# Performance work log

Measured on AMD Instinct MI355X. Metric: run time of the kernel, lower is better.

The kernel has to match this reference:

```python
import jax, jax.numpy as jnp
import numpy as np

B, T, N, D = 8, 12, 512, 128
K = 16                      # number of pattern clusters
GEO_H, SEM_H, T_H = 4, 2, 2
HD = D // (GEO_H + SEM_H + T_H)      # 16
SCALE = HD ** -0.5
GD, SD, TD = GEO_H * HD, SEM_H * HD, T_H * HD  # 64, 32, 32


def setup_inputs() -> dict:
    key = jax.random.key(0)
    ks = jax.random.split(key, 24)
    w = lambda k, o, i: jax.random.normal(k, (o, i), jnp.float32) * 0.02
    return {
        'x': jax.random.normal(ks[0], (B, T, N, D), jnp.float32),
        'x_patterns': jax.random.normal(ks[1], (B, T, N, D, 1), jnp.float32),
        'pattern_keys': jax.random.normal(ks[2], (K, D, 1), jnp.float32),
        'dynamic_adj': jax.random.normal(ks[3], (B, N, N), jnp.float32) * 0.1,
        'geo_mask': jax.random.randint(ks[4], (N, N), 0, 2).astype(bool),
        'sem_mask': jax.random.randint(ks[5], (N, N), 0, 2).astype(bool),
        't_qw': w(ks[6], TD, D), 't_kw': w(ks[7], TD, D), 't_vw': w(ks[8], TD, D),
        'geo_qw': w(ks[9], GD, D), 'geo_kw': w(ks[10], GD, D), 'geo_vw': w(ks[11], GD, D),
        'sem_qw': w(ks[12], SD, D), 'sem_kw': w(ks[13], SD, D), 'sem_vw': w(ks[14], SD, D),
        'pat_qw': w(ks[15], GD, D), 'pat_qb': jax.random.normal(ks[16], (GD,), jnp.float32) * 0.02,
        'pat_kw': w(ks[17], GD, D), 'pat_kb': jax.random.normal(ks[18], (GD,), jnp.float32) * 0.02,
        'pat_vw': w(ks[19], GD, D), 'pat_vb': jax.random.normal(ks[20], (GD,), jnp.float32) * 0.02,
        'proj_w': w(ks[21], D, D), 'proj_b': jax.random.normal(ks[22], (D,), jnp.float32) * 0.02,
    }


def reference(x, x_patterns, pattern_keys, dynamic_adj, geo_mask, sem_mask,
              t_qw, t_kw, t_vw, geo_qw, geo_kw, geo_vw, sem_qw, sem_kw, sem_vw,
              pat_qw, pat_qb, pat_kw, pat_kb, pat_vw, pat_vb, proj_w, proj_b):
    Bc, Tc, Nc, Dc = x.shape
    proj3 = lambda z, w: jnp.einsum('btnd,ed->btne', z, w)  # 1x1 conv over channels

    # ---- temporal branch: attention over T per node ----
    def t_heads(z):  # (B,T,N,TD) -> (B,N,h,T,hd)
        return z.transpose(0, 2, 1, 3).reshape(Bc, Nc, Tc, T_H, HD).transpose(0, 1, 3, 2, 4)
    tq, tk, tv = t_heads(proj3(x, t_qw)), t_heads(proj3(x, t_kw)), t_heads(proj3(x, t_vw))
    t_attn = jax.nn.softmax(jnp.einsum('bnhqd,bnhkd->bnhqk', tq, tk) * SCALE, axis=-1)
    t_x = jnp.einsum('bnhqk,bnhkd->bnhqd', t_attn, tv)
    t_x = t_x.transpose(0, 1, 3, 2, 4).reshape(Bc, Nc, Tc, TD).transpose(0, 2, 1, 3)  # (B,T,N,TD)

    # ---- geo branch: pattern attention augments geo_k ----
    geo_q, geo_k, geo_v = proj3(x, geo_qw), proj3(x, geo_kw), proj3(x, geo_vw)
    pq = x_patterns[..., 0] @ pat_qw.T + pat_qb          # (B,T,N,GD)
    pk = pattern_keys[..., 0] @ pat_kw.T + pat_kb        # (K,GD)
    pv = pattern_keys[..., 0] @ pat_vw.T + pat_vb        # (K,GD)
    p_attn = jax.nn.softmax(jnp.einsum('btne,ke->btnk', pq, pk) * SCALE, axis=-1)
    geo_k = geo_k + jnp.einsum('btnk,ke->btne', p_attn, pv)

    def s_heads(z, h):  # (B,T,N,h*hd) -> (B,T,h,N,hd)
        return z.reshape(Bc, Tc, Nc, h, HD).transpose(0, 1, 3, 2, 4)
    gq, gk, gv = s_heads(geo_q, GEO_H), s_heads(geo_k, GEO_H), s_heads(geo_v, GEO_H)
    g_attn = jnp.einsum('bthqd,bthkd->bthqk', gq, gk) * SCALE
    g_attn = g_attn + dynamic_adj[:, None, None]         # dynamic bias
    g_attn = jnp.where(geo_mask, -jnp.inf, g_attn)
    g_attn = jax.nn.softmax(g_attn, axis=-1)
    geo_x = jnp.einsum('bthqk,bthkd->bthqd', g_attn, gv)
    geo_x = geo_x.transpose(0, 1, 3, 2, 4).reshape(Bc, Tc, Nc, GD)

    # ---- semantic branch ----
    sq = s_heads(proj3(x, sem_qw), SEM_H)
    sk = s_heads(proj3(x, sem_kw), SEM_H)
    sv = s_heads(proj3(x, sem_vw), SEM_H)
    s_attn = jnp.einsum('bthqd,bthkd->bthqk', sq, sk) * SCALE
    s_attn = jnp.where(sem_mask, -jnp.inf, s_attn)
    s_attn = jax.nn.softmax(s_attn, axis=-1)
    sem_x = jnp.einsum('bthqk,bthkd->bthqd', s_attn, sv)
    sem_x = sem_x.transpose(0, 1, 3, 2, 4).reshape(Bc, Tc, Nc, SD)

    out = jnp.concatenate([t_x, geo_x, sem_x], axis=-1) @ proj_w.T + proj_b
    return out
```

## Files before the change

kernel.cpp:

```cpp
#include <hip/hip_runtime.h>
#include <hip/hip_bf16.h>

using bf16 = __hip_bfloat16;
typedef __attribute__((ext_vector_type(8))) short short8;
typedef __attribute__((ext_vector_type(4))) float f32x4;

#define Bc 8
#define Tc 12
#define Nc 512
#define Dc 128
#define T_Hc 2
#define GEO_Hc 4
#define SEM_Hc 2
#define HDc 16
#define SCALEc 0.25f

constexpr size_t TSZ = (size_t)Bc * Nc * T_Hc * Tc * HDc;
constexpr size_t GSZ = (size_t)Bc * Tc * GEO_Hc * Nc * HDc;
constexpr size_t SSZ = (size_t)Bc * Tc * SEM_Hc * Nc * HDc;
constexpr size_t CSZ = (size_t)Bc * Tc * Nc * Dc;
constexpr size_t H_TQ = 0;
constexpr size_t H_TK = H_TQ + TSZ;
constexpr size_t H_TV = H_TK + TSZ;
constexpr size_t H_GQ = H_TV + TSZ;
constexpr size_t H_GK = H_GQ + GSZ;
constexpr size_t H_GV = H_GK + GSZ;
constexpr size_t H_SQ = H_GV + GSZ;
constexpr size_t H_SK = H_SQ + SSZ;
constexpr size_t H_SV = H_SK + SSZ;
constexpr size_t H_CC = H_SV + SSZ;
constexpr size_t H_END = H_CC + CSZ;
constexpr size_t F_PK = (H_END + 1) / 2;
constexpr size_t F_PV = F_PK + 1024;
constexpr size_t F_FLAG = F_PV + 1024;
constexpr size_t H_W2X = 2 * (F_FLAG + 64);
constexpr size_t H_W2O = H_W2X + 384 * 256;
constexpr size_t H_BG = H_TQ;
constexpr size_t H_BS = H_TQ + 2097152;

__device__ __forceinline__ float b2f(bf16 v) { return __bfloat162float(v); }
__device__ __forceinline__ bf16 f2b(float v) { return __float2bfloat16(v); }
__device__ __forceinline__ short f2bs(float v) {
    bf16 b = __float2bfloat16(v);
    return *reinterpret_cast<short*>(&b);
}
__device__ __forceinline__ float bs2f(short s) {
    union { unsigned u; float f; } x;
    x.u = ((unsigned)(unsigned short)s) << 16;
    return x.f;
}

__global__ __launch_bounds__(256) void k_prep(
    const float* __restrict__ pattern_keys, const float* __restrict__ pat_kw,
    const float* __restrict__ pat_kb, const float* __restrict__ pat_vw,
    const float* __restrict__ pat_vb, float* __restrict__ fws) {
    int idx = blockIdx.x * 256 + threadIdx.x;
    int which = idx >> 10;
    int r = idx & 1023;
    int k = r >> 6, e = r & 63;
    const float4* w = (const float4*)((which ? pat_vw : pat_kw) + (size_t)e * 128);
    const float4* pk = (const float4*)(pattern_keys + (size_t)k * 128);
    float acc = which ? pat_vb[e] : pat_kb[e];
#pragma unroll
    for (int j = 0; j < 32; ++j) {
        float4 a = pk[j], b = w[j];
        acc = fmaf(a.x, b.x, acc); acc = fmaf(a.y, b.y, acc);
        acc = fmaf(a.z, b.z, acc); acc = fmaf(a.w, b.w, acc);
    }
    fws[(which ? F_PV : F_PK) + (size_t)k * 64 + e] = acc;
}

__global__ __launch_bounds__(256) void k_maskdet(
    const unsigned char* __restrict__ mask, float* __restrict__ fws) {
    __shared__ int s_u8, s_odd4;
    int tid = threadIdx.x;
    if (tid == 0) { s_u8 = 0; s_odd4 = 0; }
    __syncthreads();
    int u8 = 0, odd4 = 0;
    for (int i = tid * 16; i < tid * 16 + 16; ++i) {
        unsigned char v = mask[i];
        if (v && (i & 3)) u8 = 1;
        if (v && ((i & 7) == 4)) odd4 = 1;
    }
    if (u8) atomicOr(&s_u8, 1);
    if (odd4) atomicOr(&s_odd4, 1);
    __syncthreads();
    if (tid == 0) fws[F_FLAG] = s_u8 ? 0.f : (s_odd4 ? 1.f : 2.f);
}

__device__ __forceinline__ const float* wrow(
    int gc, const float* tq, const float* tk, const float* tv,
    const float* gq, const float* gk, const float* gv,
    const float* sq, const float* sk, const float* sv) {
    if (gc < 32) return tq + (size_t)gc * 128;
    if (gc < 64) return tk + (size_t)(gc - 32) * 128;
    if (gc < 96) return tv + (size_t)(gc - 64) * 128;
    if (gc < 160) return gq + (size_t)(gc - 96) * 128;
    if (gc < 224) return gk + (size_t)(gc - 160) * 128;
    if (gc < 288) return gv + (size_t)(gc - 224) * 128;
    if (gc < 320) return sq + (size_t)(gc - 288) * 128;
    if (gc < 352) return sk + (size_t)(gc - 320) * 128;
    return sv + (size_t)(gc - 352) * 128;
}

__global__ __launch_bounds__(256) void k_wcvt(
    const float* __restrict__ t_qw, const float* __restrict__ t_kw,
    const float* __restrict__ t_vw, const float* __restrict__ geo_qw,
    const float* __restrict__ geo_kw, const float* __restrict__ geo_vw,
    const float* __restrict__ sem_qw, const float* __restrict__ sem_kw,
    const float* __restrict__ sem_vw, const float* __restrict__ proj_w,
    bf16* __restrict__ hb) {
    int gid = blockIdx.x * 256 + threadIdx.x;
    if (gid < 49152) {
        int row = gid >> 7, k = gid & 127;
        const float* src = wrow(row, t_qw, t_kw, t_vw, geo_qw, geo_kw, geo_vw,
                                sem_qw, sem_kw, sem_vw);
        float v = src[k];
        if ((row >= 96 && row < 160) || (row >= 288 && row < 320)) v *= SCALEc;
        bf16 bv = f2b(v);
        hb[H_W2X + (size_t)row * 256 + 2 * k] = bv;
        hb[H_W2X + (size_t)row * 256 + 2 * k + 1] = bv;
    } else {
        int g = gid - 49152;
        hb[H_W2O + g] = f2b(proj_w[g]);
    }
}

__global__ __launch_bounds__(256) void k_bias(
    const float* __restrict__ dyn, const unsigned char* __restrict__ gm,
    const unsigned char* __restrict__ sm, const float* __restrict__ fws,
    bf16* __restrict__ hb) {
    size_t gid = (size_t)blockIdx.x * 256 + threadIdx.x;
    int mode = (int)fws[F_FLAG];
    if (gid < 2097152) {
        size_t rem = gid & 262143;
        int mv = (mode == 0) ? (int)gm[rem]
               : (mode == 1) ? ((const int*)gm)[rem]
                             : ((const int*)gm)[2 * rem];
        hb[H_BG + gid] = f2b(mv ? -1e30f : dyn[gid]);
    } else if (gid < 2097152 + 262144) {
        size_t sid = gid - 2097152;
        int mv = (mode == 0) ? (int)sm[sid]
               : (mode == 1) ? ((const int*)sm)[sid]
                             : ((const int*)sm)[2 * sid];
        hb[H_BS + sid] = f2b(mv ? -1e30f : 0.f);
    }
}

__global__ __launch_bounds__(256, 2) void k_projx(
    const float* __restrict__ x, bf16* __restrict__ hb) {
    __shared__ short xs[128 * 256];

    int tid = threadIdx.x;
    int m0 = blockIdx.x * 128;
    int b = m0 / (Tc * Nc);
    int rr = m0 - b * Tc * Nc;
    int t = rr >> 9;
    int n0 = rr & 511;

    for (int u = tid; u < 4096; u += 256) {
        int row = u >> 5, g = u & 31;
        float4 v = *(const float4*)(x + (size_t)(m0 + row) * 128 + g * 4);
        short8 s;
        short h0 = f2bs(v.x); s[0] = h0; s[1] = f2bs(v.x - bs2f(h0));
        short h1 = f2bs(v.y); s[2] = h1; s[3] = f2bs(v.y - bs2f(h1));
        short h2 = f2bs(v.z); s[4] = h2; s[5] = f2bs(v.z - bs2f(h2));
        short h3 = f2bs(v.w); s[6] = h3; s[7] = f2bs(v.w - bs2f(h3));
        *(short8*)&xs[row * 256 + ((g ^ (row & 7)) << 3)] = s;
    }
    __syncthreads();

    int w = tid >> 6;
    int lane = tid & 63;
    int l15 = lane & 15;
    int quad = lane >> 4;
    const bf16* w2 = hb + H_W2X;

    for (int nc = 0; nc < 6; ++nc) {
        f32x4 acc[2][4];
#pragma unroll
        for (int i = 0; i < 2; ++i)
#pragma unroll
            for (int j = 0; j < 4; ++j) acc[i][j] = (f32x4){0.f, 0.f, 0.f, 0.f};

#pragma unroll
        for (int ks = 0; ks < 8; ++ks) {
            int r0 = w * 32 + l15;
            int r1 = r0 + 16;
            short8 a0 = *(const short8*)&xs[r0 * 256 + (((ks * 4 + quad) ^ (r0 & 7)) << 3)];
            short8 a1 = *(const short8*)&xs[r1 * 256 + (((ks * 4 + quad) ^ (r1 & 7)) << 3)];
#pragma unroll
            for (int nj = 0; nj < 4; ++nj) {
                short8 bfr = *(const short8*)(w2 + (size_t)(nc * 64 + nj * 16 + l15) * 256
                                              + ks * 32 + quad * 8);
                acc[0][nj] = __builtin_amdgcn_mfma_f32_16x16x32_bf16(a0, bfr, acc[0][nj], 0, 0, 0);
                acc[1][nj] = __builtin_amdgcn_mfma_f32_16x16x32_bf16(a1, bfr, acc[1][nj], 0, 0, 0);
            }
        }
#pragma unroll
        for (int nj = 0; nj < 4; ++nj) {
            int gc = nc * 64 + nj * 16 + l15;
            int tile16 = nc * 4 + nj;
            int d = gc & 15;
#pragma unroll
            for (int i = 0; i < 2; ++i) {
                int nrow0 = n0 + w * 32 + i * 16 + quad * 4;
#pragma unroll
                for (int r = 0; r < 4; ++r) {
                    int n = nrow0 + r;
                    float v = acc[i][nj][r];
                    size_t idx;
                    if (tile16 < 6) {
                        int which = gc >> 5, hh = (gc >> 4) & 1;
                        size_t base = which == 0 ? H_TQ : which == 1 ? H_TK : H_TV;
                        idx = base + ((size_t)(b * Nc + n) * T_Hc + hh) * (Tc * HDc)
                              + t * HDc + d;
                    } else if (tile16 < 18) {
                        int r2 = gc - 96;
                        int which = r2 >> 6, h = (r2 >> 4) & 3;
                        size_t base = which == 0 ? H_GQ : which == 1 ? H_GK : H_GV;
                        idx = base + (((size_t)b * Tc + t) * GEO_Hc + h) * (Nc * HDc)
                              + n * HDc + d;
                    } else {
                        int r2 = gc - 288;
                        int which = r2 >> 5, h = (r2 >> 4) & 1;
                        size_t base = which == 0 ? H_SQ : which == 1 ? H_SK : H_SV;
                        idx = base + (((size_t)b * Tc + t) * SEM_Hc + h) * (Nc * HDc)
                              + n * HDc + d;
                    }
                    hb[idx] = f2b(v);
                }
            }
        }
    }
}

__global__ __launch_bounds__(256, 2) void k_projp(
    const float* __restrict__ xp, const float* __restrict__ pat_qw,
    const float* __restrict__ pat_qb, const float* __restrict__ fws,
    bf16* __restrict__ hb) {
    __shared__ float xs[64 * 132];
    __shared__ float wsh[64 * 68];
    __shared__ float pks[1024], pvs[1024], pqbs[64];

    int tid = threadIdx.x;
    int tok0 = blockIdx.x * 64;
    int ty = tid >> 4, tx = tid & 15;

    for (int u = tid; u < 2048; u += 256) {
        int row = u >> 5, f4 = u & 31;
        *(float4*)&xs[row * 132 + f4 * 4] =
            *(const float4*)(xp + (size_t)(tok0 + row) * 128 + f4 * 4);
    }
    for (int u = tid; u < 1024; u += 256) {
        pks[u] = fws[F_PK + u];
        pvs[u] = fws[F_PV + u];
    }
    if (tid < 64) pqbs[tid] = pat_qb[tid];

    float acc[4][4] = {};
    for (int kh = 0; kh < 2; ++kh) {
        __syncthreads();
        for (int u = tid; u < 1024; u += 256) {
            int row = u >> 4, f4 = u & 15;
            *(float4*)&wsh[row * 68 + f4 * 4] =
                *(const float4*)(pat_qw + (size_t)row * 128 + kh * 64 + f4 * 4);
        }
        __syncthreads();
#pragma unroll 4
        for (int kk = 0; kk < 64; kk += 4) {
            float4 a[4], b[4];
#pragma unroll
            for (int i = 0; i < 4; ++i)
                a[i] = *(const float4*)&xs[(ty + 16 * i) * 132 + kh * 64 + kk];
#pragma unroll
            for (int j = 0; j < 4; ++j)
                b[j] = *(const float4*)&wsh[(tx + 16 * j) * 68 + kk];
#pragma unroll
            for (int i = 0; i < 4; ++i)
#pragma unroll
                for (int j = 0; j < 4; ++j) {
                    acc[i][j] = fmaf(a[i].x, b[j].x, acc[i][j]);
                    acc[i][j] = fmaf(a[i].y, b[j].y, acc[i][j]);
                    acc[i][j] = fmaf(a[i].z, b[j].z, acc[i][j]);
                    acc[i][j] = fmaf(a[i].w, b[j].w, acc[i][j]);
                }
        }
    }
    __syncthreads();
    float* pqs = xs;
    float* plogs = wsh;
#pragma unroll
    for (int i = 0; i < 4; ++i)
#pragma unroll
        for (int j = 0; j < 4; ++j)
            pqs[(ty + 16 * i) * 68 + tx + 16 * j] = acc[i][j] + pqbs[tx + 16 * j];
    __syncthreads();
    {
        int tok = tid >> 2, k4 = (tid & 3) * 4;
        for (int k = k4; k < k4 + 4; ++k) {
            float s = 0.f;
#pragma unroll 16
            for (int e = 0; e < 64; ++e)
                s = fmaf(pqs[tok * 68 + e], pks[k * 64 + e], s);
            plogs[tok * 17 + k] = s * SCALEc;
        }
    }
    __syncthreads();
    {
        int tok = tid >> 2, q = tid & 3;
        float mx = -1e30f;
        for (int k = 0; k < 16; ++k) mx = fmaxf(mx, plogs[tok * 17 + k]);
        float p[16], sum = 0.f;
        for (int k = 0; k < 16; ++k) {
            p[k] = __expf(plogs[tok * 17 + k] - mx);
            sum += p[k];
        }
        float inv = 1.f / sum;
        int token = tok0 + tok;
        int b = token / (Tc * Nc);
        int rr = token - b * Tc * Nc;
        int t = rr >> 9;
        int n = rr & 511;
        for (int cc = 0; cc < 16; ++cc) {
            int c = q * 16 + cc;
            float v = 0.f;
            for (int k = 0; k < 16; ++k) v = fmaf(p[k], pvs[k * 64 + c], v);
            v *= inv;
            size_t idx = H_GK + (((size_t)b * Tc + t) * GEO_Hc + (c >> 4)) * (Nc * HDc)
                         + n * HDc + (c & 15);
            hb[idx] = f2b(b2f(hb[idx]) + v);
        }
    }
}

__global__ __launch_bounds__(64) void k_tattn(bf16* __restrict__ hb) {
    int blk = blockIdx.x;
    int h = blk & 1;
    int bn = blk >> 1;
    int b = bn >> 9;
    int n = bn & 511;
    size_t base = ((size_t)(b * Nc + n) * T_Hc + h) * (Tc * HDc);

    __shared__ float q[192], kk[192], v[192], s[144];
    int tid = threadIdx.x;
    for (int u = tid; u < 192; u += 64) {
        q[u] = b2f(hb[H_TQ + base + u]);
        kk[u] = b2f(hb[H_TK + base + u]);
        v[u] = b2f(hb[H_TV + base + u]);
    }
    __syncthreads();
    for (int idx = tid; idx < 144; idx += 64) {
        int qi = idx / 12, ki = idx - qi * 12;
        float acc = 0.f;
#pragma unroll
        for (int d = 0; d < 16; ++d) acc = fmaf(q[qi * 16 + d], kk[ki * 16 + d], acc);
        s[idx] = acc * SCALEc;
    }
    __syncthreads();
    if (tid < 12) {
        float mx = -1e30f;
        for (int ki = 0; ki < 12; ++ki) mx = fmaxf(mx, s[tid * 12 + ki]);
        float sum = 0.f;
        for (int ki = 0; ki < 12; ++ki) {
            float p = __expf(s[tid * 12 + ki] - mx);
            s[tid * 12 + ki] = p;
            sum += p;
        }
        float inv = 1.f / sum;
        for (int ki = 0; ki < 12; ++ki) s[tid * 12 + ki] *= inv;
    }
    __syncthreads();
    for (int idx = tid; idx < 192; idx += 64) {
        int qi = idx >> 4, d = idx & 15;
        float acc = 0.f;
#pragma unroll
        for (int ki = 0; ki < 12; ++ki) acc = fmaf(s[qi * 12 + ki], v[ki * 16 + d], acc);
        hb[H_CC + (((size_t)b * Tc + qi) * Nc + n) * Dc + h * HDc + d] = f2b(acc);
    }
}

__global__ __launch_bounds__(256, 4) void k_attn2(
    bf16* __restrict__ hb, size_t QO, size_t KO, size_t VO, int H,
    const bf16* __restrict__ biasp, size_t bstride, int coff) {
    __shared__ short vt[16 * 512];
    __shared__ short pbuf[4][16 * 128];
    __shared__ float lt[4][16];
    __shared__ float at[4][16];

    int bid = blockIdx.x;
    int part = bid & 3;
    int bth_lin = bid >> 2;
    int h = bth_lin % H;
    int rest = bth_lin / H;
    int t = rest % Tc;
    int b = rest / Tc;

    size_t bth = (((size_t)b * Tc + t) * H + h) * (size_t)(Nc * HDc);
    const bf16* Qp = hb + QO + bth;
    const bf16* Kp = hb + KO + bth;
    const bf16* Vp = hb + VO + bth;
    const bf16* bp = biasp + (size_t)b * bstride;

    int tid = threadIdx.x;
    int w = tid >> 6;
    int lane = tid & 63;
    int l15 = lane & 15;
    int quad = lane >> 4;

    for (int idx = tid; idx < 8192; idx += 256) {
        int k = idx >> 4, d = idx & 15;
        int kk = ((((k >> 3) & 7) ^ (d & 7)) << 3) | (k & ~63) | (k & 7);
        vt[d * 512 + kk] = *reinterpret_cast<const short*>(Vp + idx);
    }
    __syncthreads();

    short* pw = &pbuf[w][0];
    float* lw = lt[w];
    float* aw = at[w];
    int sw = l15 & 7;

    for (int qq = 0; qq < 2; ++qq) {
        int q0 = part * 128 + w * 32 + qq * 16;
        int qg = q0 + l15;
        short8 bq = {0, 0, 0, 0, 0, 0, 0, 0};
        if (quad < 2) bq = *(const short8*)(Qp + (size_t)qg * 16 + quad * 8);

        float m_i = -3e38f, l_i = 0.f;
        f32x4 O = {0.f, 0.f, 0.f, 0.f};

        for (int ch = 0; ch < 4; ++ch) {
            int kabs0 = ch * 128;
            f32x4 S[8];
#pragma unroll
            for (int kt = 0; kt < 8; ++kt) {
                int kabs = kabs0 + kt * 16;
                short4 bb = *(const short4*)(bp + (size_t)qg * 512 + kabs + quad * 4);
                f32x4 c;
                c[0] = bs2f(bb.x); c[1] = bs2f(bb.y);
                c[2] = bs2f(bb.z); c[3] = bs2f(bb.w);
                short8 ak = {0, 0, 0, 0, 0, 0, 0, 0};
                if (quad < 2)
                    ak = *(const short8*)(Kp + (size_t)(kabs + l15) * 16 + quad * 8);
                S[kt] = __builtin_amdgcn_mfma_f32_16x16x32_bf16(ak, bq, c, 0, 0, 0);
            }
            float cm = S[0][0];
#pragma unroll
            for (int kt = 0; kt < 8; ++kt)
#pragma unroll
                for (int r = 0; r < 4; ++r) cm = fmaxf(cm, S[kt][r]);
            cm = fmaxf(cm, __shfl_xor(cm, 16));
            cm = fmaxf(cm, __shfl_xor(cm, 32));
            float mnew = fmaxf(m_i, cm);
            float alpha = __expf(m_i - mnew);
            m_i = mnew;
            float psum = 0.f;
#pragma unroll
            for (int kt = 0; kt < 8; ++kt) {
#pragma unroll
                for (int r = 0; r < 4; ++r) {
                    float p = __expf(S[kt][r] - mnew);
                    S[kt][r] = p;
                    psum += p;
                }
            }
            psum += __shfl_xor(psum, 16);
            psum += __shfl_xor(psum, 32);
            l_i = l_i * alpha + psum;
            if (quad == 0) aw[l15] = alpha;
#pragma unroll
            for (int kt = 0; kt < 8; ++kt) {
                short4 pk4;
                pk4.x = f2bs(S[kt][0]); pk4.y = f2bs(S[kt][1]);
                pk4.z = f2bs(S[kt][2]); pk4.w = f2bs(S[kt][3]);
                int g = 2 * kt + (quad >> 1);
                *(short4*)&pw[l15 * 128 + ((g ^ sw) << 3) + ((quad & 1) << 2)] = pk4;
            }
            float4 a4 = *(float4*)&aw[quad * 4];
            O[0] *= a4.x; O[1] *= a4.y; O[2] *= a4.z; O[3] *= a4.w;
#pragma unroll
            for (int kw = 0; kw < 4; ++kw) {
                int g = 4 * kw + quad;
                short8 ap = *(const short8*)&pw[l15 * 128 + ((g ^ sw) << 3)];
                short8 bv = *(const short8*)&vt[l15 * 512 + kabs0 + ((g ^ sw) << 3)];
                O = __builtin_amdgcn_mfma_f32_16x16x32_bf16(ap, bv, O, 0, 0, 0);
            }
        }
        if (quad == 0) lw[l15] = l_i;
        float4 l4 = *(float4*)&lw[quad * 4];
        float inv0 = 1.f / l4.x, inv1 = 1.f / l4.y, inv2 = 1.f / l4.z, inv3 = 1.f / l4.w;
        size_t obase = H_CC + (((size_t)b * Tc + t) * Nc + q0) * Dc + coff + h * HDc + l15;
        hb[obase + (size_t)(quad * 4 + 0) * Dc] = f2b(O[0] * inv0);
        hb[obase + (size_t)(quad * 4 + 1) * Dc] = f2b(O[1] * inv1);
        hb[obase + (size_t)(quad * 4 + 2) * Dc] = f2b(O[2] * inv2);
        hb[obase + (size_t)(quad * 4 + 3) * Dc] = f2b(O[3] * inv3);
    }
}

__global__ __launch_bounds__(256, 3) void k_outm(
    const bf16* __restrict__ hb, const float* __restrict__ proj_b,
    float* __restrict__ out) {
    __shared__ short cs[128 * 128];
    __shared__ float pbs[128];

    int tid = threadIdx.x;
    int m0 = blockIdx.x * 128;

    for (int u = tid; u < 2048; u += 256) {
        int row = u >> 4, g = u & 15;
        *(short8*)&cs[row * 128 + ((g ^ (row & 7)) << 3)] =
            *(const short8*)(hb + H_CC + (size_t)(m0 + row) * 128 + g * 8);
    }
    if (tid < 128) pbs[tid] = proj_b[tid];
    __syncthreads();

    int w = tid >> 6;
    int lane = tid & 63;
    int l15 = lane & 15;
    int quad = lane >> 4;
    const bf16* w2o = hb + H_W2O;

    f32x4 acc[2][8];
#pragma unroll
    for (int i = 0; i < 2; ++i)
#pragma unroll
        for (int j = 0; j < 8; ++j) acc[i][j] = (f32x4){0.f, 0.f, 0.f, 0.f};

#pragma unroll
    for (int ks = 0; ks < 4; ++ks) {
        int r0 = w * 32 + l15;
        int r1 = r0 + 16;
        short8 a0 = *(const short8*)&cs[r0 * 128 + (((ks * 4 + quad) ^ (r0 & 7)) << 3)];
        short8 a1 = *(const short8*)&cs[r1 * 128 + (((ks * 4 + quad) ^ (r1 & 7)) << 3)];
#pragma unroll
        for (int nj = 0; nj < 8; ++nj) {
            short8 bfr = *(const short8*)(w2o + (size_t)(nj * 16 + l15) * 128
                                          + ks * 32 + quad * 8);
            acc[0][nj] = __builtin_amdgcn_mfma_f32_16x16x32_bf16(a0, bfr, acc[0][nj], 0, 0, 0);
            acc[1][nj] = __builtin_amdgcn_mfma_f32_16x16x32_bf16(a1, bfr, acc[1][nj], 0, 0, 0);
        }
    }
#pragma unroll
    for (int i = 0; i < 2; ++i) {
#pragma unroll
        for (int nj = 0; nj < 8; ++nj) {
            int ch = nj * 16 + l15;
            float bias = pbs[ch];
#pragma unroll
            for (int r = 0; r < 4; ++r) {
                int token = m0 + w * 32 + i * 16 + quad * 4 + r;
                out[(size_t)token * 128 + ch] = acc[i][nj][r] + bias;
            }
        }
    }
}

extern "C" void kernel_launch(void* const* d_in, const int* in_sizes, int n_in,
                              void* d_out, int out_size, void* d_ws, size_t ws_size,
                              hipStream_t stream) {
    const float* x = (const float*)d_in[0];
    const float* xp = (const float*)d_in[1];
    const float* pattern_keys = (const float*)d_in[2];
    const float* dyn = (const float*)d_in[3];
    const void* geo_mask = d_in[4];
    const void* sem_mask = d_in[5];
    const float* t_qw = (const float*)d_in[6];
    const float* t_kw = (const float*)d_in[7];
    const float* t_vw = (const float*)d_in[8];
    const float* geo_qw = (const float*)d_in[9];
    const float* geo_kw = (const float*)d_in[10];
    const float* geo_vw = (const float*)d_in[11];
    const float* sem_qw = (const float*)d_in[12];
    const float* sem_kw = (const float*)d_in[13];
    const float* sem_vw = (const float*)d_in[14];
    const float* pat_qw = (const float*)d_in[15];
    const float* pat_qb = (const float*)d_in[16];
    const float* pat_kw = (const float*)d_in[17];
    const float* pat_kb = (const float*)d_in[18];
    const float* pat_vw = (const float*)d_in[19];
    const float* pat_vb = (const float*)d_in[20];
    const float* proj_w = (const float*)d_in[21];
    const float* proj_b = (const float*)d_in[22];

    bf16* hb = (bf16*)d_ws;
    float* fws = (float*)d_ws;

    k_prep<<<8, 256, 0, stream>>>(pattern_keys, pat_kw, pat_kb, pat_vw, pat_vb, fws);
    k_maskdet<<<1, 256, 0, stream>>>((const unsigned char*)geo_mask, fws);
    k_wcvt<<<256, 256, 0, stream>>>(t_qw, t_kw, t_vw, geo_qw, geo_kw, geo_vw,
                                    sem_qw, sem_kw, sem_vw, proj_w, hb);
    k_projx<<<384, 256, 0, stream>>>(x, hb);
    k_projp<<<768, 256, 0, stream>>>(xp, pat_qw, pat_qb, fws, hb);
    k_tattn<<<Bc * Nc * T_Hc, 64, 0, stream>>>(hb);
    k_bias<<<9216, 256, 0, stream>>>(dyn, (const unsigned char*)geo_mask,
                                     (const unsigned char*)sem_mask, fws, hb);
    k_attn2<<<Bc * Tc * GEO_Hc * 4, 256, 0, stream>>>(
        hb, H_GQ, H_GK, H_GV, GEO_Hc, hb + H_BG, (size_t)Nc * Nc, 32);
    k_attn2<<<Bc * Tc * SEM_Hc * 4, 256, 0, stream>>>(
        hb, H_SQ, H_SK, H_SV, SEM_Hc, hb + H_BS, 0, 96);
    k_outm<<<384, 256, 0, stream>>>(hb, proj_b, (float*)d_out);
}
```

Baseline: 366.6 us.

## Write V transposed in projection and merge geo/sem attention into one launch

The projection kernel now stores V for the geo and semantic heads transposed (d-major), so the attention kernel reads V fragments straight from global memory. This removes the per-block LDS staging of V and its barrier. The two attention launches are merged into a single kernel with a block-index swizzle. Alpha and row-sum broadcasts move from LDS to lane shuffles, and occupancy bounds are raised. The risk is that repeated global/L2 reads of V replace cheap LDS reads, and the projection writes to V become strided.

```diff
diff --git a/kernel.cpp b/kernel.cpp
--- a/kernel.cpp
+++ b/kernel.cpp
@@ -217,16 +217,18 @@
                               + t * HDc + d;
                     } else if (tile16 < 18) {
                         int r2 = gc - 96;
-                        int which = r2 >> 6, h = (r2 >> 4) & 3;
+                        int which = r2 >> 6, hh = (r2 >> 4) & 3;
                         size_t base = which == 0 ? H_GQ : which == 1 ? H_GK : H_GV;
-                        idx = base + (((size_t)b * Tc + t) * GEO_Hc + h) * (Nc * HDc)
-                              + n * HDc + d;
+                        size_t sl = (((size_t)b * Tc + t) * GEO_Hc + hh) * (Nc * HDc);
+                        idx = base + sl + (which == 2 ? ((size_t)d * Nc + n)
+                                                      : ((size_t)n * HDc + d));
                     } else {
                         int r2 = gc - 288;
-                        int which = r2 >> 5, h = (r2 >> 4) & 1;
+                        int which = r2 >> 5, hh = (r2 >> 4) & 1;
                         size_t base = which == 0 ? H_SQ : which == 1 ? H_SK : H_SV;
-                        idx = base + (((size_t)b * Tc + t) * SEM_Hc + h) * (Nc * HDc)
-                              + n * HDc + d;
+                        size_t sl = (((size_t)b * Tc + t) * SEM_Hc + hh) * (Nc * HDc);
+                        idx = base + sl + (which == 2 ? ((size_t)d * Nc + n)
+                                                      : ((size_t)n * HDc + d));
                     }
                     hb[idx] = f2b(v);
                 }
@@ -380,17 +382,24 @@
     }
 }
 
-__global__ __launch_bounds__(256, 4) void k_attn2(
-    bf16* __restrict__ hb, size_t QO, size_t KO, size_t VO, int H,
-    const bf16* __restrict__ biasp, size_t bstride, int coff) {
-    __shared__ short vt[16 * 512];
+__global__ __launch_bounds__(256, 6) void k_attn2m(bf16* __restrict__ hb) {
     __shared__ short pbuf[4][16 * 128];
-    __shared__ float lt[4][16];
-    __shared__ float at[4][16];
-
-    int bid = blockIdx.x;
-    int part = bid & 3;
-    int bth_lin = bid >> 2;
+
+    int bid0 = blockIdx.x;
+    int swz = (bid0 & 7) * 288 + (bid0 >> 3);
+
+    int H, coff, lb;
+    size_t QO, KO, VO, bstride;
+    const bf16* bias0;
+    if (swz < 1536) {
+        H = GEO_Hc; coff = 32; QO = H_GQ; KO = H_GK; VO = H_GV;
+        bias0 = hb + H_BG; bstride = (size_t)Nc * Nc; lb = swz;
+    } else {
+        H = SEM_Hc; coff = 96; QO = H_SQ; KO = H_SK; VO = H_SV;
+        bias0 = hb + H_BS; bstride = 0; lb = swz - 1536;
+    }
+    int part = lb & 3;
+    int bth_lin = lb >> 2;
     int h = bth_lin % H;
     int rest = bth_lin / H;
     int t = rest % Tc;
@@ -399,25 +408,15 @@
     size_t bth = (((size_t)b * Tc + t) * H + h) * (size_t)(Nc * HDc);
     const bf16* Qp = hb + QO + bth;
     const bf16* Kp = hb + KO + bth;
-    const bf16* Vp = hb + VO + bth;
-    const bf16* bp = biasp + (size_t)b * bstride;
+    const bf16* Vt = hb + VO + bth;
+    const bf16* bp = bias0 + (size_t)b * bstride;
 
     int tid = threadIdx.x;
     int w = tid >> 6;
     int lane = tid & 63;
     int l15 = lane & 15;
     int quad = lane >> 4;
-
-    for (int idx = tid; idx < 8192; idx += 256) {
-        int k = idx >> 4, d = idx & 15;
-        int kk = ((((k >> 3) & 7) ^ (d & 7)) << 3) | (k & ~63) | (k & 7);
-        vt[d * 512 + kk] = *reinterpret_cast<const short*>(Vp + idx);
-    }
-    __syncthreads();
-
     short* pw = &pbuf[w][0];
-    float* lw = lt[w];
-    float* aw = at[w];
     int sw = l15 & 7;
 
     for (int qq = 0; qq < 2; ++qq) {
@@ -467,7 +466,6 @@
             psum += __shfl_xor(psum, 16);
             psum += __shfl_xor(psum, 32);
             l_i = l_i * alpha + psum;
-            if (quad == 0) aw[l15] = alpha;
 #pragma unroll
             for (int kt = 0; kt < 8; ++kt) {
                 short4 pk4;
@@ -476,24 +474,28 @@
                 int g = 2 * kt + (quad >> 1);
                 *(short4*)&pw[l15 * 128 + ((g ^ sw) << 3) + ((quad & 1) << 2)] = pk4;
             }
-            float4 a4 = *(float4*)&aw[quad * 4];
-            O[0] *= a4.x; O[1] *= a4.y; O[2] *= a4.z; O[3] *= a4.w;
+            float a0 = __shfl(alpha, (quad << 2) | 0);
+            float a1 = __shfl(alpha, (quad << 2) | 1);
+            float a2 = __shfl(alpha, (quad << 2) | 2);
+            float a3 = __shfl(alpha, (quad << 2) | 3);
+            O[0] *= a0; O[1] *= a1; O[2] *= a2; O[3] *= a3;
 #pragma unroll
             for (int kw = 0; kw < 4; ++kw) {
                 int g = 4 * kw + quad;
                 short8 ap = *(const short8*)&pw[l15 * 128 + ((g ^ sw) << 3)];
-                short8 bv = *(const short8*)&vt[l15 * 512 + kabs0 + ((g ^ sw) << 3)];
+                short8 bv = *(const short8*)(Vt + (size_t)l15 * 512 + kabs0 + (g << 3));
                 O = __builtin_amdgcn_mfma_f32_16x16x32_bf16(ap, bv, O, 0, 0, 0);
             }
         }
-        if (quad == 0) lw[l15] = l_i;
-        float4 l4 = *(float4*)&lw[quad * 4];
-        float inv0 = 1.f / l4.x, inv1 = 1.f / l4.y, inv2 = 1.f / l4.z, inv3 = 1.f / l4.w;
+        float li0 = __shfl(l_i, (quad << 2) | 0);
+        float li1 = __shfl(l_i, (quad << 2) | 1);
+        float li2 = __shfl(l_i, (quad << 2) | 2);
+        float li3 = __shfl(l_i, (quad << 2) | 3);
         size_t obase = H_CC + (((size_t)b * Tc + t) * Nc + q0) * Dc + coff + h * HDc + l15;
-        hb[obase + (size_t)(quad * 4 + 0) * Dc] = f2b(O[0] * inv0);
-        hb[obase + (size_t)(quad * 4 + 1) * Dc] = f2b(O[1] * inv1);
-        hb[obase + (size_t)(quad * 4 + 2) * Dc] = f2b(O[2] * inv2);
-        hb[obase + (size_t)(quad * 4 + 3) * Dc] = f2b(O[3] * inv3);
+        hb[obase + (size_t)(quad * 4 + 0) * Dc] = f2b(O[0] / li0);
+        hb[obase + (size_t)(quad * 4 + 1) * Dc] = f2b(O[1] / li1);
+        hb[obase + (size_t)(quad * 4 + 2) * Dc] = f2b(O[2] / li2);
+        hb[obase + (size_t)(quad * 4 + 3) * Dc] = f2b(O[3] / li3);
     }
 }
 
@@ -594,9 +596,6 @@
     k_tattn<<<Bc * Nc * T_Hc, 64, 0, stream>>>(hb);
     k_bias<<<9216, 256, 0, stream>>>(dyn, (const unsigned char*)geo_mask,
                                      (const unsigned char*)sem_mask, fws, hb);
-    k_attn2<<<Bc * Tc * GEO_Hc * 4, 256, 0, stream>>>(
-        hb, H_GQ, H_GK, H_GV, GEO_Hc, hb + H_BG, (size_t)Nc * Nc, 32);
-    k_attn2<<<Bc * Tc * SEM_Hc * 4, 256, 0, stream>>>(
-        hb, H_SQ, H_SK, H_SV, SEM_Hc, hb + H_BS, 0, 96);
+    k_attn2m<<<Bc * Tc * (GEO_Hc + SEM_Hc) * 4, 256, 0, stream>>>(hb);
     k_outm<<<384, 256, 0, stream>>>(hb, proj_b, (float*)d_out);
 }
```

Result: slower. 385.6 us (+5.2%).
